# Kernel optimization log

Measured on AMD Instinct MI355X. Metric: run time of the kernel, lower is better.

Reference implementation:

```python
import jax, jax.numpy as jnp
import numpy as np

DIM = 1536
NH = 12
HD = DIM // NH          # 128
C = HD // 2             # 64 complex freq slots per head
DT = C - 2 * (C // 3)   # 22 temporal
DS = C // 3             # 21 per spatial axis
EPS = 1e-6
M_TAB = 64              # rope table length (>= max(f,h,w))


def _rope_tables():
    def tab(d):
        inv = 1.0 / (10000.0 ** (np.arange(d, dtype=np.float64) / d))
        ang = np.outer(np.arange(M_TAB, dtype=np.float64), inv)
        return np.cos(ang), np.sin(ang)
    ct, st = tab(DT)
    ch, sh = tab(DS)
    cw, sw = tab(DS)
    fc = np.concatenate([ct, ch, cw], axis=1).astype(np.float32)  # [M, 64]
    fs = np.concatenate([st, sh, sw], axis=1).astype(np.float32)
    return jnp.asarray(fc), jnp.asarray(fs)


def setup_inputs() -> dict:
    key = jax.random.key(0)
    ks = jax.random.split(key, 6)
    B, F, H, W = 1, 8, 22, 40
    L = F * H * W  # 7040
    s = 0.02
    x = jax.random.normal(ks[0], (B, L, DIM), jnp.float32)
    Wq = jax.random.normal(ks[1], (DIM, DIM), jnp.float32) * s
    Wk = jax.random.normal(ks[2], (DIM, DIM), jnp.float32) * s
    Wv = jax.random.normal(ks[3], (DIM, DIM), jnp.float32) * s
    Wo = jax.random.normal(ks[4], (DIM, DIM), jnp.float32) * s
    bk2 = jax.random.split(ks[5], 4)
    bq = jax.random.normal(bk2[0], (DIM,), jnp.float32) * s
    bk = jax.random.normal(bk2[1], (DIM,), jnp.float32) * s
    bv = jax.random.normal(bk2[2], (DIM,), jnp.float32) * s
    bo = jax.random.normal(bk2[3], (DIM,), jnp.float32) * s
    fc, fs = _rope_tables()
    return dict(x=x, Wq=Wq, bq=bq, Wk=Wk, bk=bk, Wv=Wv, bv=bv, Wo=Wo, bo=bo,
                gq=jnp.ones((DIM,), jnp.float32), gk=jnp.ones((DIM,), jnp.float32),
                freqs_cos=fc, freqs_sin=fs,
                num_frames=F, grid_h=H, grid_w=W,
                chunk_size=2, sink_size=1, max_attention_size=2640)


def _pos_table(tab, f, h, w):
    # tab: [M, 64] -> per-token [f*h*w, 64] via (t,h,w) axis split [22,21,21]
    t = jnp.broadcast_to(tab[:f, :DT][:, None, None, :], (f, h, w, DT))
    hh = jnp.broadcast_to(tab[:h, DT:DT + DS][None, :, None, :], (f, h, w, DS))
    ww = jnp.broadcast_to(tab[:w, DT + DS:][None, None, :, :], (f, h, w, DS))
    return jnp.concatenate([t, hh, ww], axis=-1).reshape(f * h * w, C)


def _forward(x, Wq, bq, Wk, bk, Wv, bv, Wo, bo, gq, gk, freqs_cos, freqs_sin,
             num_frames, grid_h, grid_w, chunk_size, sink_size, max_attention_size):
    B, L, D = x.shape
    lin = lambda t, W, b: jnp.einsum('bld,ed->ble', t, W) + b
    rms = lambda t, g: t * jax.lax.rsqrt(jnp.mean(t * t, axis=-1, keepdims=True) + EPS) * g

    q = rms(lin(x, Wq, bq), gq).reshape(B, L, NH, HD)
    k = rms(lin(x, Wk, bk), gk).reshape(B, L, NH, HD)
    v = lin(x, Wv, bv).reshape(B, L, NH, HD)

    # causal RoPE (start_frame=0)
    cosL = _pos_table(freqs_cos, num_frames, grid_h, grid_w)  # [L, 64]
    sinL = _pos_table(freqs_sin, num_frames, grid_h, grid_w)

    def rope(t):
        a = t.reshape(B, L, NH, C, 2)
        xr, xi = a[..., 0], a[..., 1]
        co = cosL[None, :, None, :]
        si = sinL[None, :, None, :]
        return jnp.stack([xr * co - xi * si, xr * si + xi * co], axis=-1).reshape(B, L, NH, HD)

    q = rope(q)
    k = rope(k)

    # loop attention, diffusion forcing: chunk i attends [0,(i+1)*block) with sink+window
    frame_seqlen = grid_h * grid_w
    block = frame_seqlen * chunk_size
    total_len = num_frames * frame_seqlen
    sink_end = sink_size * frame_seqlen
    num_chunks = -(-total_len // block)
    scale = 1.0 / (HD ** 0.5)

    def attn(qi, ki, vi):
        s = jnp.einsum('bqnd,bknd->bnqk', qi, ki) * scale
        p = jax.nn.softmax(s, axis=-1)
        return jnp.einsum('bnqk,bknd->bqnd', p, vi)

    outs = []
    for i in range(num_chunks):
        q_start = i * block
        q_end = min((i + 1) * block, total_len)
        qi = q[:, q_start:q_end]
        chunk_end = q_end
        if max_attention_size == -1 or sink_end == 0:
            if max_attention_size == -1:
                ki, vi = k[:, :chunk_end], v[:, :chunk_end]
            else:
                ws = max(0, chunk_end - max_attention_size)
                ki, vi = k[:, ws:chunk_end], v[:, ws:chunk_end]
        else:
            window = max_attention_size - sink_end
            ws = max(sink_end, chunk_end - window)
            ki = jnp.concatenate([k[:, :sink_end], k[:, ws:chunk_end]], axis=1)
            vi = jnp.concatenate([v[:, :sink_end], v[:, ws:chunk_end]], axis=1)
        outs.append(attn(qi, ki, vi))

    o = jnp.concatenate(outs, axis=1).reshape(B, L, D)
    return jnp.einsum('bld,ed->ble', o, Wo) + bo


def reference(x, Wq, bq, Wk, bk, Wv, bv, Wo, bo, gq, gk, freqs_cos, freqs_sin,
              num_frames, grid_h, grid_w, chunk_size, sink_size, max_attention_size):
    return _forward(x, Wq, bq, Wk, bk, Wv, bv, Wo, bo, gq, gk, freqs_cos, freqs_sin,
                    num_frames, grid_h, grid_w, chunk_size, sink_size, max_attention_size)
```

## Files before the change

### kernel.cpp

```cpp
#include <hip/hip_runtime.h>
#include <math.h>

typedef __attribute__((ext_vector_type(8))) short short8;
typedef __attribute__((ext_vector_type(4))) float f32x4;
typedef __attribute__((ext_vector_type(16))) float f32x16;
typedef __attribute__((ext_vector_type(4))) float f4;
typedef __attribute__((ext_vector_type(4))) unsigned short us4;
typedef __attribute__((ext_vector_type(2))) unsigned int u32x2;

#define MFMA16(a,b,c) __builtin_amdgcn_mfma_f32_16x16x32_bf16(a,b,c,0,0,0)
#define MFMA32(a,b,c) __builtin_amdgcn_mfma_f32_32x32x16_bf16(a,b,c,0,0,0)

__device__ __forceinline__ unsigned short f2bf(float f) {
  unsigned int u = __float_as_uint(f);
  u = (u + 0x7FFFu + ((u >> 16) & 1u)) >> 16;
  return (unsigned short)u;
}
__device__ __forceinline__ float bf2f(unsigned short b) {
  return __uint_as_float(((unsigned int)b) << 16);
}
__device__ __forceinline__ unsigned int pk2(float a, float b) {
  unsigned int au = __float_as_uint(a) + 0x8000u;
  unsigned int bu = __float_as_uint(b) + 0x8000u;
  return __builtin_amdgcn_perm(bu, au, 0x07060302u);
}

typedef const __attribute__((address_space(1))) unsigned int* gas_t;
typedef __attribute__((address_space(3))) unsigned int* las_t;
__device__ __forceinline__ void gl16(const void* g, void* l) {
  __builtin_amdgcn_global_load_lds((gas_t)g, (las_t)l, 16, 0, 0);
}

__global__ void cvt_f32_bf16(const float* __restrict__ in,
                             unsigned short* __restrict__ out, int n4) {
  int i = blockIdx.x * blockDim.x + threadIdx.x;
  const int stride = gridDim.x * blockDim.x;
  for (; i < n4; i += stride) {
    f4 v = ((const f4*)in)[i];
    us4 o;
    o[0] = f2bf(v[0]); o[1] = f2bf(v[1]); o[2] = f2bf(v[2]); o[3] = f2bf(v[3]);
    ((us4*)out)[i] = o;
  }
}

template<int F32OUT>
__global__ __launch_bounds__(256)
void gemm_bt(const unsigned short* __restrict__ A,
             const unsigned short* __restrict__ B,
             const float* __restrict__ bias,
             unsigned short* __restrict__ obf,
             float* __restrict__ of32,
             int K, int ldo)
{
  const int tid = threadIdx.x;
  const int wave = tid >> 6, lane = tid & 63, lg = lane >> 4, lr = lane & 15;
  const int wr = wave >> 1, wc = wave & 1;
  const int m0 = blockIdx.y * 128, n0 = blockIdx.x * 128;

  __shared__ __align__(16) unsigned short Al[128 * 32];
  __shared__ __align__(16) unsigned short Bl[128 * 32];

  f32x4 acc[4][4];
#pragma unroll
  for (int m = 0; m < 4; ++m)
#pragma unroll
    for (int n = 0; n < 4; ++n) acc[m][n] = (f32x4){0.f, 0.f, 0.f, 0.f};

  const int r0 = tid >> 2, r1 = (tid + 256) >> 2;
  const int c0 = (tid & 3) * 8;
  const long arow0 = (long)(m0 + r0) * K, arow1 = (long)(m0 + r1) * K;
  const long brow0 = (long)(n0 + r0) * K, brow1 = (long)(n0 + r1) * K;

  for (int k0 = 0; k0 < K; k0 += 32) {
    gl16(A + arow0 + k0 + c0, (char*)Al + tid * 16);
    gl16(A + arow1 + k0 + c0, (char*)Al + (tid + 256) * 16);
    gl16(B + brow0 + k0 + c0, (char*)Bl + tid * 16);
    gl16(B + brow1 + k0 + c0, (char*)Bl + (tid + 256) * 16);
    __syncthreads();
    short8 af[4], bf[4];
#pragma unroll
    for (int m = 0; m < 4; ++m)
      af[m] = *(const short8*)(Al + (wr * 64 + m * 16 + lr) * 32 + lg * 8);
#pragma unroll
    for (int n = 0; n < 4; ++n)
      bf[n] = *(const short8*)(Bl + (wc * 64 + n * 16 + lr) * 32 + lg * 8);
#pragma unroll
    for (int m = 0; m < 4; ++m)
#pragma unroll
      for (int n = 0; n < 4; ++n)
        acc[m][n] = MFMA16(af[m], bf[n], acc[m][n]);
    __syncthreads();
  }

#pragma unroll
  for (int n = 0; n < 4; ++n) {
    const int col = n0 + wc * 64 + n * 16 + lr;
    const float bs = bias[col];
#pragma unroll
    for (int m = 0; m < 4; ++m) {
      const int row = m0 + wr * 64 + m * 16 + lg * 4;
#pragma unroll
      for (int r = 0; r < 4; ++r) {
        float v = acc[m][n][r] + bs;
        if (F32OUT) of32[(long)(row + r) * ldo + col] = v;
        else        obf[(long)(row + r) * ldo + col] = f2bf(v);
      }
    }
  }
}

__global__ __launch_bounds__(256)
void normrope(unsigned short* __restrict__ qkv, const float* __restrict__ g,
              const float* __restrict__ fc, const float* __restrict__ fs,
              int colOff, float oscale)
{
  const int l = blockIdx.x, tid = threadIdx.x;
  __shared__ float rowbuf[1536];
  __shared__ float sred[4];
  unsigned short* rp = qkv + (long)l * 4608 + colOff;

  float ss = 0.f;
  if (tid < 192) {
    short8 v = *(const short8*)(rp + tid * 8);
#pragma unroll
    for (int e = 0; e < 8; ++e) {
      float f = bf2f((unsigned short)v[e]);
      rowbuf[tid * 8 + e] = f;
      ss += f * f;
    }
  }
#pragma unroll
  for (int m = 32; m; m >>= 1) ss += __shfl_xor(ss, m, 64);
  if ((tid & 63) == 0) sred[tid >> 6] = ss;
  __syncthreads();
  const float rs = rsqrtf((sred[0] + sred[1] + sred[2] + sred[3]) * (1.f / 1536.f) + 1e-6f);

  const int f_ = l / 880, rem = l % 880, h_ = rem / 40, w_ = rem % 40;
#pragma unroll
  for (int j = 0; j < 3; ++j) {
    int p = tid + j * 256;
    int head = p >> 6, c = p & 63;
    int e = head * 128 + 2 * c;
    int tr = (c < 22) ? f_ : ((c < 43) ? h_ : w_);
    float co = fc[tr * 64 + c], si = fs[tr * 64 + c];
    float xr = rowbuf[e] * rs * g[e];
    float xi = rowbuf[e + 1] * rs * g[e + 1];
    float yr = (xr * co - xi * si) * oscale;
    float yi = (xr * si + xi * co) * oscale;
    unsigned int pk = (unsigned int)f2bf(yr) | ((unsigned int)f2bf(yi) << 16);
    *(unsigned int*)(rp + e) = pk;
  }
}

__device__ __forceinline__ void issueK(const unsigned short* __restrict__ qkv,
                                       int h, int t, int kvlen, int woff, int tid,
                                       unsigned short* Kbuf)
{
#pragma unroll
  for (int i = 0; i < 4; ++i) {
    int s = i * 256 + tid;
    int kvl = s >> 4;
    int dc = (s & 15) ^ (kvl & 7);
    int j = t * 64 + kvl; j = j < kvlen ? j : kvlen - 1;
    int gk = j + (j >= 880 ? woff : 0);
    gl16(qkv + (long)gk * 4608 + 1536 + h * 128 + dc * 8, (char*)Kbuf + s * 16);
  }
}

__device__ __forceinline__ void loadV(const unsigned short* __restrict__ qkv,
                                      int h, int t, int kvlen, int woff, int tid,
                                      short8 vp[2][2])
{
#pragma unroll
  for (int i = 0; i < 2; ++i) {
    int task = i * 256 + tid;
    int dc = task & 15, kp = task >> 4;
    int kvl = kp * 2;
    int j0 = t * 64 + kvl, j1 = j0 + 1;
    j0 = j0 < kvlen ? j0 : kvlen - 1;
    j1 = j1 < kvlen ? j1 : kvlen - 1;
    int g0 = j0 + (j0 >= 880 ? woff : 0);
    int g1 = j1 + (j1 >= 880 ? woff : 0);
    vp[i][0] = *(const short8*)(qkv + (long)g0 * 4608 + 3072 + h * 128 + dc * 8);
    vp[i][1] = *(const short8*)(qkv + (long)g1 * 4608 + 3072 + h * 128 + dc * 8);
  }
}

__device__ __forceinline__ void writeV(int tid, short8 vp[2][2], unsigned short* Vt)
{
#pragma unroll
  for (int i = 0; i < 2; ++i) {
    int task = i * 256 + tid;
    int dc = task & 15, kp = task >> 4;
    int kvl = kp * 2;
#pragma unroll
    for (int e = 0; e < 8; ++e) {
      int d = dc * 8 + e;
      int byte = d * 128 + kvl * 2;
      byte ^= (((d & 7) ^ ((d >> 3) & 7)) << 4);
      *(unsigned int*)((char*)Vt + byte) =
          (unsigned int)(unsigned short)vp[i][0][e] |
          ((unsigned int)(unsigned short)vp[i][1][e] << 16);
    }
  }
}

__global__ __launch_bounds__(256, 2)
void attn_kern(const unsigned short* __restrict__ qkv,
               unsigned short* __restrict__ ob)
{
  const int qt = blockIdx.x, ci = blockIdx.y, h = blockIdx.z;
  const int tid = threadIdx.x, wave = tid >> 6, lane = tid & 63;
  const int l31 = lane & 31, hh = lane >> 5;
  const int chunk_start = ci * 1760, chunk_end = chunk_start + 1760;
  const int wstart = (ci == 0) ? 880 : ci * 1760;
  const int woff = wstart - 880;
  const int kvlen = 880 + (chunk_end - wstart);
  const int q0 = chunk_start + qt * 128;

  __shared__ __align__(16) unsigned short Kl[2][64 * 128];
  __shared__ __align__(16) unsigned short Vt[2][128 * 64];

  int qr = q0 + wave * 32 + l31;
  if (qr >= chunk_end) qr = chunk_end - 1;
  const unsigned short* qp = qkv + (long)qr * 4608 + h * 128;
  short8 qf[8];
#pragma unroll
  for (int st = 0; st < 8; ++st) qf[st] = *(const short8*)(qp + st * 16 + hh * 8);

  f32x16 Oc[4];
#pragma unroll
  for (int i = 0; i < 4; ++i)
#pragma unroll
    for (int j = 0; j < 16; ++j) Oc[i][j] = 0.f;
  float m_run = -1e30f, l_run = 0.f;
  unsigned int w0[8], w1[8];

  auto computeQK = [&](int t, int cur, f32x16* S0, f32x16* S1) {
    f32x16 a0, a1;
#pragma unroll
    for (int j = 0; j < 16; ++j) { a0[j] = 0.f; a1[j] = 0.f; }
    __builtin_amdgcn_s_setprio(1);
#pragma unroll
    for (int st = 0; st < 8; ++st) {
      int off = 32 * st + 16 * hh;
      int b0 = l31 * 256 + (off ^ ((l31 & 7) << 4));
      short8 k0 = *(const short8*)((const char*)&Kl[cur][0] + b0);
      a0 = MFMA32(k0, qf[st], a0);
      int b1 = (32 + l31) * 256 + (off ^ ((l31 & 7) << 4));
      short8 k1 = *(const short8*)((const char*)&Kl[cur][0] + b1);
      a1 = MFMA32(k1, qf[st], a1);
    }
    __builtin_amdgcn_s_setprio(0);
    if (t * 64 + 64 > kvlen) {
#pragma unroll
      for (int r = 0; r < 16; ++r) {
        int kv0 = t * 64 + (r & 3) + 8 * (r >> 2) + 4 * hh;
        if (kv0 >= kvlen)      a0[r] = -1e30f;
        if (kv0 + 32 >= kvlen) a1[r] = -1e30f;
      }
    }
    *S0 = a0; *S1 = a1;
  };

  auto finishTile = [&](f32x16& s0f, f32x16& s1f) {
    float mx[16];
#pragma unroll
    for (int r = 0; r < 16; ++r) mx[r] = fmaxf(s0f[r], s1f[r]);
#pragma unroll
    for (int w = 8; w; w >>= 1)
#pragma unroll
      for (int r = 0; r < w; ++r) mx[r] = fmaxf(mx[r], mx[r + w]);
    float pm = fmaxf(mx[0], __shfl_xor(mx[0], 32, 64));
    const bool defer = __all(pm <= m_run + 8.f);
    const float mn = defer ? m_run : fmaxf(m_run, pm);
#pragma unroll
    for (int r = 0; r < 16; ++r) {
      s0f[r] = __builtin_amdgcn_exp2f(s0f[r] - mn);
      s1f[r] = __builtin_amdgcn_exp2f(s1f[r] - mn);
    }
    float sm[16];
#pragma unroll
    for (int r = 0; r < 16; ++r) sm[r] = s0f[r] + s1f[r];
#pragma unroll
    for (int w = 8; w; w >>= 1)
#pragma unroll
      for (int r = 0; r < w; ++r) sm[r] += sm[r + w];
    float sum = sm[0] + __shfl_xor(sm[0], 32, 64);
    if (defer) {
      l_run += sum;
    } else {
      float al = __builtin_amdgcn_exp2f(m_run - mn);
      l_run = l_run * al + sum;
      m_run = mn;
#pragma unroll
      for (int i = 0; i < 4; ++i)
#pragma unroll
        for (int j = 0; j < 16; ++j) Oc[i][j] *= al;
    }
#pragma unroll
    for (int m = 0; m < 8; ++m) {
      w0[m] = pk2(s0f[2 * m], s0f[2 * m + 1]);
      w1[m] = pk2(s1f[2 * m], s1f[2 * m + 1]);
    }
  };

  auto doPV = [&](int cur) {
    __builtin_amdgcn_s_setprio(1);
#pragma unroll
    for (int s = 0; s < 4; ++s) {
      const unsigned int* w = (s < 2) ? w0 : w1;
      const int lo4 = (s & 1) * 4;
      unsigned int x0 = __shfl_xor(w[lo4 + 2], 32, 64);
      unsigned int x1 = __shfl_xor(w[lo4 + 3], 32, 64);
      unsigned int y0 = __shfl_xor(w[lo4],     32, 64);
      unsigned int y1 = __shfl_xor(w[lo4 + 1], 32, 64);
      unsigned int fw[4];
      fw[0] = hh ? x0 : w[lo4];
      fw[1] = hh ? x1 : w[lo4 + 1];
      fw[2] = hh ? w[lo4 + 2] : y0;
      fw[3] = hh ? w[lo4 + 3] : y1;
      short8 pb = *(const short8*)fw;
#pragma unroll
      for (int dt = 0; dt < 4; ++dt) {
        int d = dt * 32 + l31;
        int byte = d * 128 + s * 32 + hh * 16;
        byte ^= (((d & 7) ^ ((d >> 3) & 7)) << 4);
        short8 vf = *(const short8*)((const char*)&Vt[cur][0] + byte);
        Oc[dt] = MFMA32(vf, pb, Oc[dt]);
      }
    }
    __builtin_amdgcn_s_setprio(0);
  };

  const int nt = (kvlen + 63) >> 6;
  short8 vp[2][2];

  issueK(qkv, h, 0, kvlen, woff, tid, &Kl[0][0]);
  if (nt > 1) issueK(qkv, h, 1, kvlen, woff, tid, &Kl[1][0]);
  loadV(qkv, h, 0, kvlen, woff, tid, vp);
  writeV(tid, vp, &Vt[0][0]);
  __syncthreads();

  f32x16 sp0, sp1;
  computeQK(0, 0, &sp0, &sp1);
  __syncthreads();

  for (int t = 0; t < nt - 1; ++t) {
    const int cur = t & 1;
    if (t + 2 < nt) issueK(qkv, h, t + 2, kvlen, woff, tid, &Kl[cur][0]);
    loadV(qkv, h, t + 1, kvlen, woff, tid, vp);

    f32x16 sc0, sc1;
    computeQK(t + 1, cur ^ 1, &sc0, &sc1);
    finishTile(sp0, sp1);
    writeV(tid, vp, &Vt[cur ^ 1][0]);
    doPV(cur);
    __syncthreads();
    sp0 = sc0; sp1 = sc1;
  }
  finishTile(sp0, sp1);
  doPV((nt - 1) & 1);

  const int qg = q0 + wave * 32 + l31;
  if (qg < chunk_end) {
    const float inv = 1.f / l_run;
    unsigned short* op = ob + (long)qg * 1536 + h * 128;
#pragma unroll
    for (int dt = 0; dt < 4; ++dt) {
#pragma unroll
      for (int gblk = 0; gblk < 4; ++gblk) {
        int d = dt * 32 + gblk * 8 + hh * 4;
        unsigned int u0 = pk2(Oc[dt][4 * gblk]     * inv, Oc[dt][4 * gblk + 1] * inv);
        unsigned int u1 = pk2(Oc[dt][4 * gblk + 2] * inv, Oc[dt][4 * gblk + 3] * inv);
        u32x2 uu; uu[0] = u0; uu[1] = u1;
        *(u32x2*)(op + d) = uu;
      }
    }
  }
}

extern "C" void kernel_launch(void* const* d_in, const int* in_sizes, int n_in,
                              void* d_out, int out_size, void* d_ws, size_t ws_size,
                              hipStream_t stream)
{
  const float* x  = (const float*)d_in[0];
  const float* Wq = (const float*)d_in[1];
  const float* bq = (const float*)d_in[2];
  const float* Wk = (const float*)d_in[3];
  const float* bk = (const float*)d_in[4];
  const float* Wv = (const float*)d_in[5];
  const float* bv = (const float*)d_in[6];
  const float* Wo = (const float*)d_in[7];
  const float* bo = (const float*)d_in[8];
  const float* gq = (const float*)d_in[9];
  const float* gk = (const float*)d_in[10];
  const float* fc = (const float*)d_in[11];
  const float* fs = (const float*)d_in[12];

  char* ws = (char*)d_ws;
  unsigned short* xb   = (unsigned short*)(ws);
  unsigned short* wcat = (unsigned short*)(ws + 21626880);
  unsigned short* wob  = (unsigned short*)(ws + 35782656);
  float*          bcat = (float*)(ws + 40501248);
  unsigned short* qkv  = (unsigned short*)(ws + 40519680);
  unsigned short* obuf = (unsigned short*)(ws + 105400320);

  cvt_f32_bf16<<<2048, 256, 0, stream>>>(x,  xb,   10813440 / 4);
  cvt_f32_bf16<<<1024, 256, 0, stream>>>(Wq, wcat,            2359296 / 4);
  cvt_f32_bf16<<<1024, 256, 0, stream>>>(Wk, wcat + 2359296,  2359296 / 4);
  cvt_f32_bf16<<<1024, 256, 0, stream>>>(Wv, wcat + 4718592,  2359296 / 4);
  cvt_f32_bf16<<<1024, 256, 0, stream>>>(Wo, wob,             2359296 / 4);
  hipMemcpyAsync(bcat,        bq, 1536 * 4, hipMemcpyDeviceToDevice, stream);
  hipMemcpyAsync(bcat + 1536, bk, 1536 * 4, hipMemcpyDeviceToDevice, stream);
  hipMemcpyAsync(bcat + 3072, bv, 1536 * 4, hipMemcpyDeviceToDevice, stream);

  gemm_bt<0><<<dim3(36, 55), 256, 0, stream>>>(xb, wcat, bcat, qkv, nullptr, 1536, 4608);

  const float qsc = (float)(1.4426950408889634 / sqrt(128.0));
  normrope<<<7040, 256, 0, stream>>>(qkv, gq, fc, fs, 0,    qsc);
  normrope<<<7040, 256, 0, stream>>>(qkv, gk, fc, fs, 1536, 1.0f);

  attn_kern<<<dim3(14, 4, 12), 256, 0, stream>>>(qkv, obuf);

  gemm_bt<1><<<dim3(12, 55), 256, 0, stream>>>(obuf, wob, bo, nullptr, (float*)d_out, 1536, 1536);
}
```

Measured before the change: 442.5 us.

## Pre-transpose V globally and stream it into LDS with async loads

Adds a separate kernel that writes V into a head-dim-major [1536 x 7040] buffer (reusing the bf16 x workspace). The attention kernel then fills its V tile with direct global-to-LDS loads, the same way it fills K. This replaces the register staging and scattered 32-bit LDS transpose writes done on every tile. The cost is an extra launch plus one full read and write of V, and a simpler XOR swizzle on the V reads.

```diff
diff --git a/kernel.cpp b/kernel.cpp
--- a/kernel.cpp
+++ b/kernel.cpp
@@ -40,6 +40,34 @@
     us4 o;
     o[0] = f2bf(v[0]); o[1] = f2bf(v[1]); o[2] = f2bf(v[2]); o[3] = f2bf(v[3]);
     ((us4*)out)[i] = o;
+  }
+}
+
+__global__ __launch_bounds__(256)
+void vtrans(const unsigned short* __restrict__ qkv, unsigned short* __restrict__ vt)
+{
+  __shared__ unsigned int tile[64][65];
+  const int lb = blockIdx.x * 64;
+  const int rb = blockIdx.y * 64;
+  const int tid = threadIdx.x;
+
+#pragma unroll
+  for (int i = 0; i < 2; ++i) {
+    int task = i * 256 + tid;
+    int l = task >> 3, c = task & 7;
+    short8 v = *(const short8*)(qkv + (long)(lb + l) * 4608 + 3072 + rb + c * 8);
+#pragma unroll
+    for (int e = 0; e < 8; ++e) tile[c * 8 + e][l] = (unsigned short)v[e];
+  }
+  __syncthreads();
+#pragma unroll
+  for (int i = 0; i < 2; ++i) {
+    int task = i * 256 + tid;
+    int r = task >> 3, c = task & 7;
+    short8 o;
+#pragma unroll
+    for (int e = 0; e < 8; ++e) o[e] = (short)tile[r][c * 8 + e];
+    *(short8*)(vt + (long)(rb + r) * 7040 + lb + c * 8) = o;
   }
 }
 
@@ -167,46 +195,25 @@
   }
 }
 
-__device__ __forceinline__ void loadV(const unsigned short* __restrict__ qkv,
-                                      int h, int t, int kvlen, int woff, int tid,
-                                      short8 vp[2][2])
-{
-#pragma unroll
-  for (int i = 0; i < 2; ++i) {
-    int task = i * 256 + tid;
-    int dc = task & 15, kp = task >> 4;
-    int kvl = kp * 2;
-    int j0 = t * 64 + kvl, j1 = j0 + 1;
-    j0 = j0 < kvlen ? j0 : kvlen - 1;
-    j1 = j1 < kvlen ? j1 : kvlen - 1;
-    int g0 = j0 + (j0 >= 880 ? woff : 0);
-    int g1 = j1 + (j1 >= 880 ? woff : 0);
-    vp[i][0] = *(const short8*)(qkv + (long)g0 * 4608 + 3072 + h * 128 + dc * 8);
-    vp[i][1] = *(const short8*)(qkv + (long)g1 * 4608 + 3072 + h * 128 + dc * 8);
-  }
-}
-
-__device__ __forceinline__ void writeV(int tid, short8 vp[2][2], unsigned short* Vt)
-{
-#pragma unroll
-  for (int i = 0; i < 2; ++i) {
-    int task = i * 256 + tid;
-    int dc = task & 15, kp = task >> 4;
-    int kvl = kp * 2;
-#pragma unroll
-    for (int e = 0; e < 8; ++e) {
-      int d = dc * 8 + e;
-      int byte = d * 128 + kvl * 2;
-      byte ^= (((d & 7) ^ ((d >> 3) & 7)) << 4);
-      *(unsigned int*)((char*)Vt + byte) =
-          (unsigned int)(unsigned short)vp[i][0][e] |
-          ((unsigned int)(unsigned short)vp[i][1][e] << 16);
-    }
+__device__ __forceinline__ void issueV(const unsigned short* __restrict__ vt,
+                                       int h, int t, int kvlen, int woff, int tid,
+                                       unsigned short* Vbuf)
+{
+#pragma unroll
+  for (int i = 0; i < 4; ++i) {
+    int s = i * 256 + tid;
+    int d = s >> 3;
+    int c = (s & 7) ^ (d & 7);
+    int j = t * 64 + c * 8;
+    j = j < kvlen ? j : kvlen - 8;
+    int gk = j + (j >= 880 ? woff : 0);
+    gl16(vt + (long)(h * 128 + d) * 7040 + gk, (char*)Vbuf + s * 16);
   }
 }
 
 __global__ __launch_bounds__(256, 2)
 void attn_kern(const unsigned short* __restrict__ qkv,
+               const unsigned short* __restrict__ vt,
                unsigned short* __restrict__ ob)
 {
   const int qt = blockIdx.x, ci = blockIdx.y, h = blockIdx.z;
@@ -324,8 +331,7 @@
 #pragma unroll
       for (int dt = 0; dt < 4; ++dt) {
         int d = dt * 32 + l31;
-        int byte = d * 128 + s * 32 + hh * 16;
-        byte ^= (((d & 7) ^ ((d >> 3) & 7)) << 4);
+        int byte = (d * 128 + s * 32 + hh * 16) ^ ((d & 7) << 4);
         short8 vf = *(const short8*)((const char*)&Vt[cur][0] + byte);
         Oc[dt] = MFMA32(vf, pb, Oc[dt]);
       }
@@ -334,12 +340,10 @@
   };
 
   const int nt = (kvlen + 63) >> 6;
-  short8 vp[2][2];
 
   issueK(qkv, h, 0, kvlen, woff, tid, &Kl[0][0]);
   if (nt > 1) issueK(qkv, h, 1, kvlen, woff, tid, &Kl[1][0]);
-  loadV(qkv, h, 0, kvlen, woff, tid, vp);
-  writeV(tid, vp, &Vt[0][0]);
+  issueV(vt, h, 0, kvlen, woff, tid, &Vt[0][0]);
   __syncthreads();
 
   f32x16 sp0, sp1;
@@ -349,12 +353,11 @@
   for (int t = 0; t < nt - 1; ++t) {
     const int cur = t & 1;
     if (t + 2 < nt) issueK(qkv, h, t + 2, kvlen, woff, tid, &Kl[cur][0]);
-    loadV(qkv, h, t + 1, kvlen, woff, tid, vp);
+    issueV(vt, h, t + 1, kvlen, woff, tid, &Vt[cur ^ 1][0]);
 
     f32x16 sc0, sc1;
     computeQK(t + 1, cur ^ 1, &sc0, &sc1);
     finishTile(sp0, sp1);
-    writeV(tid, vp, &Vt[cur ^ 1][0]);
     doPV(cur);
     __syncthreads();
     sp0 = sc0; sp1 = sc1;
@@ -405,6 +408,7 @@
   float*          bcat = (float*)(ws + 40501248);
   unsigned short* qkv  = (unsigned short*)(ws + 40519680);
   unsigned short* obuf = (unsigned short*)(ws + 105400320);
+  unsigned short* vtb  = xb;
 
   cvt_f32_bf16<<<2048, 256, 0, stream>>>(x,  xb,   10813440 / 4);
   cvt_f32_bf16<<<1024, 256, 0, stream>>>(Wq, wcat,            2359296 / 4);
@@ -417,11 +421,13 @@
 
   gemm_bt<0><<<dim3(36, 55), 256, 0, stream>>>(xb, wcat, bcat, qkv, nullptr, 1536, 4608);
 
+  vtrans<<<dim3(110, 24), 256, 0, stream>>>(qkv, vtb);
+
   const float qsc = (float)(1.4426950408889634 / sqrt(128.0));
   normrope<<<7040, 256, 0, stream>>>(qkv, gq, fc, fs, 0,    qsc);
   normrope<<<7040, 256, 0, stream>>>(qkv, gk, fc, fs, 1536, 1.0f);
 
-  attn_kern<<<dim3(14, 4, 12), 256, 0, stream>>>(qkv, obuf);
+  attn_kern<<<dim3(14, 4, 12), 256, 0, stream>>>(qkv, vtb, obuf);
 
   gemm_bt<1><<<dim3(12, 55), 256, 0, stream>>>(obuf, wob, bo, nullptr, (float*)d_out, 1536, 1536);
 }
```

Result: slower. 454.6 us (+2.7%).

## Merge weight-convert and norm-rope launches, add XCD-aware GEMM tile swizzle

Applied to the files above, without the earlier changes.

The four weight conversion launches become one kernel with a 2D grid, and the Q and K norm-rope launches become one launch selected by blockIdx.y. Both GEMMs now use a 1D grid remapped so that consecutive tiles land on the same XCD (blocks are assumed to be dispatched round-robin over 8 XCDs). The goals are fewer launches and better L2 reuse of A/B tiles within each XCD. The remap relies on the round-robin dispatch assumption and adds a few integer operations per block.

```diff
diff --git a/kernel.cpp b/kernel.cpp
--- a/kernel.cpp
+++ b/kernel.cpp
@@ -43,6 +43,23 @@
   }
 }
 
+__global__ void cvt4_f32_bf16(const float* __restrict__ w0, const float* __restrict__ w1,
+                              const float* __restrict__ w2, const float* __restrict__ w3,
+                              unsigned short* __restrict__ o0, unsigned short* __restrict__ o1,
+                              unsigned short* __restrict__ o2, unsigned short* __restrict__ o3,
+                              int n4) {
+  const float* in = (blockIdx.y == 0) ? w0 : (blockIdx.y == 1) ? w1 : (blockIdx.y == 2) ? w2 : w3;
+  unsigned short* out = (blockIdx.y == 0) ? o0 : (blockIdx.y == 1) ? o1 : (blockIdx.y == 2) ? o2 : o3;
+  int i = blockIdx.x * blockDim.x + threadIdx.x;
+  const int stride = gridDim.x * blockDim.x;
+  for (; i < n4; i += stride) {
+    f4 v = ((const f4*)in)[i];
+    us4 o;
+    o[0] = f2bf(v[0]); o[1] = f2bf(v[1]); o[2] = f2bf(v[2]); o[3] = f2bf(v[3]);
+    ((us4*)out)[i] = o;
+  }
+}
+
 template<int F32OUT>
 __global__ __launch_bounds__(256)
 void gemm_bt(const unsigned short* __restrict__ A,
@@ -50,12 +67,16 @@
              const float* __restrict__ bias,
              unsigned short* __restrict__ obf,
              float* __restrict__ of32,
-             int K, int ldo)
-{
+             int K, int ldo, int nbx, int q, int r)
+{
+  const int lin = blockIdx.x;
+  const int xcd = lin & 7, local = lin >> 3;
+  const int wg = (xcd < r) ? (xcd * (q + 1) + local) : (r * (q + 1) + (xcd - r) * q + local);
+  const int m0 = (wg / nbx) * 128, n0 = (wg % nbx) * 128;
+
   const int tid = threadIdx.x;
   const int wave = tid >> 6, lane = tid & 63, lg = lane >> 4, lr = lane & 15;
   const int wr = wave >> 1, wc = wave & 1;
-  const int m0 = blockIdx.y * 128, n0 = blockIdx.x * 128;
 
   __shared__ __align__(16) unsigned short Al[128 * 32];
   __shared__ __align__(16) unsigned short Bl[128 * 32];
@@ -100,21 +121,25 @@
     for (int m = 0; m < 4; ++m) {
       const int row = m0 + wr * 64 + m * 16 + lg * 4;
 #pragma unroll
-      for (int r = 0; r < 4; ++r) {
-        float v = acc[m][n][r] + bs;
-        if (F32OUT) of32[(long)(row + r) * ldo + col] = v;
-        else        obf[(long)(row + r) * ldo + col] = f2bf(v);
+      for (int r2 = 0; r2 < 4; ++r2) {
+        float v = acc[m][n][r2] + bs;
+        if (F32OUT) of32[(long)(row + r2) * ldo + col] = v;
+        else        obf[(long)(row + r2) * ldo + col] = f2bf(v);
       }
     }
   }
 }
 
 __global__ __launch_bounds__(256)
-void normrope(unsigned short* __restrict__ qkv, const float* __restrict__ g,
+void normrope(unsigned short* __restrict__ qkv, const float* __restrict__ gq,
+              const float* __restrict__ gk,
               const float* __restrict__ fc, const float* __restrict__ fs,
-              int colOff, float oscale)
+              float qsc)
 {
   const int l = blockIdx.x, tid = threadIdx.x;
+  const int colOff = blockIdx.y ? 1536 : 0;
+  const float* g = blockIdx.y ? gk : gq;
+  const float oscale = blockIdx.y ? 1.0f : qsc;
   __shared__ float rowbuf[1536];
   __shared__ float sred[4];
   unsigned short* rp = qkv + (long)l * 4608 + colOff;
@@ -406,22 +431,22 @@
   unsigned short* qkv  = (unsigned short*)(ws + 40519680);
   unsigned short* obuf = (unsigned short*)(ws + 105400320);
 
-  cvt_f32_bf16<<<2048, 256, 0, stream>>>(x,  xb,   10813440 / 4);
-  cvt_f32_bf16<<<1024, 256, 0, stream>>>(Wq, wcat,            2359296 / 4);
-  cvt_f32_bf16<<<1024, 256, 0, stream>>>(Wk, wcat + 2359296,  2359296 / 4);
-  cvt_f32_bf16<<<1024, 256, 0, stream>>>(Wv, wcat + 4718592,  2359296 / 4);
-  cvt_f32_bf16<<<1024, 256, 0, stream>>>(Wo, wob,             2359296 / 4);
+  cvt_f32_bf16<<<2048, 256, 0, stream>>>(x, xb, 10813440 / 4);
+  cvt4_f32_bf16<<<dim3(576, 4), 256, 0, stream>>>(
+      Wq, Wk, Wv, Wo,
+      wcat, wcat + 2359296, wcat + 4718592, wob, 2359296 / 4);
   hipMemcpyAsync(bcat,        bq, 1536 * 4, hipMemcpyDeviceToDevice, stream);
   hipMemcpyAsync(bcat + 1536, bk, 1536 * 4, hipMemcpyDeviceToDevice, stream);
   hipMemcpyAsync(bcat + 3072, bv, 1536 * 4, hipMemcpyDeviceToDevice, stream);
 
-  gemm_bt<0><<<dim3(36, 55), 256, 0, stream>>>(xb, wcat, bcat, qkv, nullptr, 1536, 4608);
+  gemm_bt<0><<<1980, 256, 0, stream>>>(xb, wcat, bcat, qkv, nullptr, 1536, 4608,
+                                       36, 1980 / 8, 1980 % 8);
 
   const float qsc = (float)(1.4426950408889634 / sqrt(128.0));
-  normrope<<<7040, 256, 0, stream>>>(qkv, gq, fc, fs, 0,    qsc);
-  normrope<<<7040, 256, 0, stream>>>(qkv, gk, fc, fs, 1536, 1.0f);
+  normrope<<<dim3(7040, 2), 256, 0, stream>>>(qkv, gq, gk, fc, fs, qsc);
 
   attn_kern<<<dim3(14, 4, 12), 256, 0, stream>>>(qkv, obuf);
 
-  gemm_bt<1><<<dim3(12, 55), 256, 0, stream>>>(obuf, wob, bo, nullptr, (float*)d_out, 1536, 1536);
-}
+  gemm_bt<1><<<660, 256, 0, stream>>>(obuf, wob, bo, nullptr, (float*)d_out, 1536, 1536,
+                                      12, 660 / 8, 660 % 8);
+}
```

Measured after the change: 439.1 us. No clear change (-0.8%).
